# Kernel optimization log

Hardware: AMD Instinct MI355X
Metric: run time of the kernel (lower is better)

## Reference

```python
import jax, jax.numpy as jnp
import numpy as np

E, H, F = 1024, 16, 4096
WH, WW = 32, 32
B = 4
L = WH * WW           # 1024 cross-attn kv tokens
N = L + 1             # 1025 decoder tokens (CLS + window)
D = E // H
SCALE = D ** -0.5
NEG = -1e9            # stands in for -inf in the causal mask


def _rel_coords(Wh, Ww):
    coords = np.stack(np.meshgrid(np.arange(Wh), np.arange(Ww), indexing='ij')).reshape(2, -1)
    rc = (coords[:, :, None] - coords[:, None, :]).transpose(1, 2, 0).astype(np.int64)
    rc[:, :, 0] += Wh - 1
    rc[:, :, 1] += Ww - 1
    rc[:, :, 0] *= 2 * Ww - 1
    return rc.sum(-1)  # (L, L)


def rel_index_self(Wh, Ww):
    nrd = (2 * Wh - 1) * (2 * Ww - 1) + 3
    l = Wh * Ww
    idx = np.zeros((l + 1, l + 1), dtype=np.int32)
    idx[1:, 1:] = _rel_coords(Wh, Ww)
    idx[0, :] = nrd - 3
    idx[:, 0] = nrd - 2
    idx[0, 0] = nrd - 1
    return idx


def rel_index_cross(Wh, Ww):
    nrd = (2 * Wh - 1) * (2 * Ww - 1) + 1
    l = Wh * Ww
    idx = np.zeros((l + 1, l), dtype=np.int32)
    idx[1:, :] = _rel_coords(Wh, Ww)
    idx[0, :] = nrd - 1
    return idx


IDX_SELF = jnp.asarray(rel_index_self(WH, WW))    # (N, N) int32
IDX_CROSS = jnp.asarray(rel_index_cross(WH, WW))  # (N, L) int32
CAUSAL = jnp.triu(jnp.full((N, N), NEG, jnp.float32), 1)


def _ln(x, g, b, eps=1e-5):
    m = x.mean(-1, keepdims=True)
    v = ((x - m) ** 2).mean(-1, keepdims=True)
    return (x - m) * jax.lax.rsqrt(v + eps) * g + b


def setup_inputs():
    key = jax.random.key(0)
    ks = jax.random.split(key, 24)
    g = lambda i, shape, s=0.02: jax.random.normal(ks[i], shape, jnp.float32) * s
    return dict(
        x=g(0, (B, N, E), 1.0),
        y=g(1, (B, L, E), 1.0),
        norm1_g=jnp.ones((E,), jnp.float32), norm1_b=jnp.zeros((E,), jnp.float32),
        norm2_g=jnp.ones((E,), jnp.float32), norm2_b=jnp.zeros((E,), jnp.float32),
        norm3_g=jnp.ones((E,), jnp.float32), norm3_b=jnp.zeros((E,), jnp.float32),
        sa_qkv_w=g(2, (3 * E, E)),
        sa_q_bias=g(3, (E,)),
        sa_v_bias=g(4, (E,)),
        sa_rpb=g(5, ((2 * WH - 1) * (2 * WW - 1) + 3, H)),
        sa_proj_w=g(6, (E, E)), sa_proj_b=g(7, (E,)),
        ca_q_w=g(8, (E, E)),
        ca_kv_w=g(9, (2 * E, E)),
        ca_q_bias=g(10, (E,)),
        ca_v_bias=g(11, (E,)),
        ca_rpb=g(12, ((2 * WH - 1) * (2 * WW - 1) + 1, H)),
        ca_proj_w=g(13, (E, E)), ca_proj_b=g(14, (E,)),
        fc1_w=g(15, (F, E)), fc1_b=g(16, (F,)),
        fc2_w=g(17, (E, F)), fc2_b=g(18, (E,)),
        gamma1=jnp.full((E,), 0.1, jnp.float32),
        gamma2=jnp.full((E,), 0.1, jnp.float32),
        gamma3=jnp.full((E,), 0.1, jnp.float32),
    )


def reference(x, y, norm1_g, norm1_b, norm2_g, norm2_b, norm3_g, norm3_b,
              sa_qkv_w, sa_q_bias, sa_v_bias, sa_rpb, sa_proj_w, sa_proj_b,
              ca_q_w, ca_kv_w, ca_q_bias, ca_v_bias, ca_rpb, ca_proj_w, ca_proj_b,
              fc1_w, fc1_b, fc2_w, fc2_b, gamma1, gamma2, gamma3):
    # cross_attn.extract_kv(y): k gets zero bias, v gets v_bias
    kv_bias = jnp.concatenate([jnp.zeros((E,), x.dtype), ca_v_bias])
    kv = (y @ ca_kv_w.T + kv_bias).reshape(B, L, 2, H, D)
    ck = kv[:, :, 0].transpose(0, 2, 1, 3)  # (B,H,L,D)
    cv = kv[:, :, 1].transpose(0, 2, 1, 3)

    # --- causal self-attention with gathered relative-position bias ---
    h = _ln(x, norm1_g, norm1_b)
    qkv_bias = jnp.concatenate([sa_q_bias, jnp.zeros((E,), x.dtype), sa_v_bias])
    qkv = (h @ sa_qkv_w.T + qkv_bias).reshape(B, N, 3, H, D)
    q = qkv[:, :, 0].transpose(0, 2, 1, 3) * SCALE  # (B,H,N,D)
    k = qkv[:, :, 1].transpose(0, 2, 1, 3)
    v = qkv[:, :, 2].transpose(0, 2, 1, 3)
    bias = sa_rpb[IDX_SELF].transpose(2, 0, 1) + CAUSAL  # (H,N,N)
    attn = jnp.einsum('bhqd,bhkd->bhqk', q, k) + bias[None]
    attn = jax.nn.softmax(attn, axis=-1)
    sa = jnp.einsum('bhqk,bhkd->bhqd', attn, v).transpose(0, 2, 1, 3).reshape(B, N, E)
    sa = sa @ sa_proj_w.T + sa_proj_b
    x = x + gamma1 * sa

    # --- cross-attention with gathered relative-position bias ---
    h = _ln(x, norm2_g, norm2_b)
    q = (h @ ca_q_w.T + ca_q_bias).reshape(B, N, H, D).transpose(0, 2, 1, 3) * SCALE
    cbias = ca_rpb[IDX_CROSS].transpose(2, 0, 1)  # (H,N,L)
    attn = jnp.einsum('bhqd,bhkd->bhqk', q, ck) + cbias[None]
    attn = jax.nn.softmax(attn, axis=-1)
    ca = jnp.einsum('bhqk,bhkd->bhqd', attn, cv).transpose(0, 2, 1, 3).reshape(B, N, E)
    ca = ca @ ca_proj_w.T + ca_proj_b
    x = x + gamma2 * ca

    # --- FFN (Linear -> GELU -> Linear, no inner identity) ---
    h = _ln(x, norm3_g, norm3_b)
    h = jax.nn.gelu(h @ fc1_w.T + fc1_b, approximate=False)
    h = h @ fc2_w.T + fc2_b
    x = x + gamma3 * h
    return x
```

## Files before the change

### kernel.cpp

```cpp
#include <hip/hip_runtime.h>
#include <hip/hip_bf16.h>
#include <math.h>

typedef __bf16 bf16;
typedef __bf16 bf16x8 __attribute__((ext_vector_type(8)));
typedef float f32x4 __attribute__((ext_vector_type(4)));

#define MP    4224
#define MACT  4100
#define NQTOK 1025
#define NKTOK 1024
#define EDIM  1024
#define FDIM  4096
#define NHEAD 16
#define HD    64
#define QSCALE 0.125f
#define VTS   1056

__device__ __forceinline__ void glds16(const bf16* g, bf16* l) {
  __builtin_amdgcn_global_load_lds(
      (const __attribute__((address_space(1))) void*)g,
      (__attribute__((address_space(3))) void*)l, 16, 0, 0);
}

__device__ __forceinline__ bf16x8 ld8(const void* p, size_t i, bool f32) {
  if (f32) {
    const float* q = (const float*)p + i;
    bf16x8 r;
#pragma unroll
    for (int j = 0; j < 8; ++j) r[j] = (bf16)q[j];
    return r;
  }
  return *(const bf16x8*)((const bf16*)p + i);
}

struct WPtrs { const float* s[8]; };
__global__ __launch_bounds__(256) void conv_kernel(WPtrs wp, bf16* dst) {
  const size_t sz[8] = {3145728UL, 1048576UL, 1048576UL, 2097152UL,
                        1048576UL, 4194304UL, 4194304UL, 4194304UL};
  size_t id = ((size_t)blockIdx.x * 256 + threadIdx.x) * 8;
  size_t off = 0;
#pragma unroll
  for (int i = 0; i < 8; ++i) {
    if (id < off + sz[i]) {
      const float* s = wp.s[i] + (id - off);
      bf16x8 r;
#pragma unroll
      for (int j = 0; j < 8; ++j) r[j] = (bf16)s[j];
      *(bf16x8*)(dst + id) = r;
      return;
    }
    off += sz[i];
  }
}

__global__ void zero_pads_kernel(bf16* hln) {
  int i = blockIdx.x * 256 + threadIdx.x;
  const int n = (MP - MACT) * EDIM;
  if (i < n) hln[(size_t)MACT * EDIM + i] = (bf16)0.0f;
}

template<bool FIRST>
__global__ __launch_bounds__(256) void ln_kernel(const float* __restrict__ src,
    float* __restrict__ xf, bf16* __restrict__ out,
    const float* __restrict__ g, const float* __restrict__ bta) {
  const int row = blockIdx.x;
  const int tid = threadIdx.x;
  float v[4];
#pragma unroll
  for (int i = 0; i < 4; ++i) {
    v[i] = src[(size_t)row * EDIM + tid + i * 256];
    if (FIRST) xf[(size_t)row * EDIM + tid + i * 256] = v[i];
  }
  float s = 0.f, sq = 0.f;
#pragma unroll
  for (int i = 0; i < 4; ++i) { s += v[i]; sq += v[i] * v[i]; }
#pragma unroll
  for (int m = 32; m >= 1; m >>= 1) {
    s += __shfl_xor(s, m);
    sq += __shfl_xor(sq, m);
  }
  __shared__ float ss[4], ssq[4];
  const int wave = tid >> 6;
  if ((tid & 63) == 0) { ss[wave] = s; ssq[wave] = sq; }
  __syncthreads();
  s = ss[0] + ss[1] + ss[2] + ss[3];
  sq = ssq[0] + ssq[1] + ssq[2] + ssq[3];
  const float mean = s * (1.f / EDIM);
  const float var = sq * (1.f / EDIM) - mean * mean;
  const float rstd = rsqrtf(var + 1e-5f);
#pragma unroll
  for (int i = 0; i < 4; ++i) {
    int e = tid + i * 256;
    out[(size_t)row * EDIM + e] = (bf16)((v[i] - mean) * rstd * g[e] + bta[e]);
  }
}

__global__ __launch_bounds__(256) void fc2_reduce_kernel(
    const float* __restrict__ p0, const float* __restrict__ xf,
    const float* __restrict__ bias, const float* __restrict__ gamma,
    float* __restrict__ outf) {
  size_t i = ((size_t)blockIdx.x * 256 + threadIdx.x) * 4;
  if (i >= (size_t)MACT * EDIM) return;
  f32x4 a = *(const f32x4*)(p0 + i);
  f32x4 b = *(const f32x4*)(outf + i);
  f32x4 x = *(const f32x4*)(xf + i);
  const int gn = (int)(i & (EDIM - 1));
  f32x4 r;
#pragma unroll
  for (int j = 0; j < 4; ++j)
    r[j] = x[j] + gamma[gn + j] * (a[j] + b[j] + bias[gn + j]);
  *(f32x4*)(outf + i) = r;
}

enum { EPI_QKV = 0, EPI_KV = 1, EPI_Q = 2, EPI_RES = 3, EPI_GELU = 4,
       EPI_FINAL = 5, EPI_PART = 6 };

template<int EPI, bool ASY>
__global__ __launch_bounds__(256) void gemm_bt(
    const void* __restrict__ A, const void* __restrict__ Bw,
    int K, int Kc,
    const float* __restrict__ bias0, const float* __restrict__ bias1,
    const float* __restrict__ gamma, float* __restrict__ xf,
    bf16* __restrict__ out0, bf16* __restrict__ out1, bf16* __restrict__ out2,
    float* __restrict__ outf)
{
  constexpr int LDP = ASY ? 32 : 40;
  __shared__ bf16 As[128][LDP];
  __shared__ bf16 Bs[128][LDP];
  const int tid = threadIdx.x;
  const int lane = tid & 63, wave = tid >> 6;
  const int quad = lane >> 4, l16 = lane & 15;
  const int wr = wave >> 1, wc = wave & 1;
  const int m0 = blockIdx.y * 128, n0 = blockIdx.x * 128;
  const int kbase = blockIdx.z * Kc;
  const bool first = (blockIdx.z == 0);
  const int r0 = tid >> 2, c0 = (tid & 3) * 8;

  const bf16* gA = nullptr; const bf16* gB = nullptr;
  bf16* lA = nullptr; bf16* lB = nullptr;
  if (ASY) {
    gA = (const bf16*)A + (size_t)(m0 + wave * 16 + (lane >> 2)) * K + kbase + (lane & 3) * 8;
    gB = (const bf16*)Bw + (size_t)(n0 + wave * 16 + (lane >> 2)) * K + kbase + (lane & 3) * 8;
    lA = &As[wave * 16][0];
    lB = &Bs[wave * 16][0];
  }

  f32x4 acc[4][4];
#pragma unroll
  for (int i = 0; i < 4; ++i)
#pragma unroll
    for (int j = 0; j < 4; ++j)
#pragma unroll
      for (int r = 0; r < 4; ++r) acc[i][j][r] = 0.f;

  for (int k0 = 0; k0 < Kc; k0 += 32) {
    if (ASY) {
      glds16(gA, lA);
      glds16(gA + (size_t)64 * K, lA + 64 * 32);
      glds16(gB, lB);
      glds16(gB + (size_t)64 * K, lB + 64 * 32);
      gA += 32; gB += 32;
    } else {
      const bool f32a = (EPI == EPI_KV);
      const size_t kk = (size_t)(kbase + k0);
      *(bf16x8*)(&As[r0][c0])      = ld8(A,  (size_t)(m0 + r0) * K + kk + c0, f32a);
      *(bf16x8*)(&As[r0 + 64][c0]) = ld8(A,  (size_t)(m0 + r0 + 64) * K + kk + c0, f32a);
      *(bf16x8*)(&Bs[r0][c0])      = ld8(Bw, (size_t)(n0 + r0) * K + kk + c0, true);
      *(bf16x8*)(&Bs[r0 + 64][c0]) = ld8(Bw, (size_t)(n0 + r0 + 64) * K + kk + c0, true);
    }
    __syncthreads();
    bf16x8 af[4], bfv[4];
#pragma unroll
    for (int i = 0; i < 4; ++i) {
      af[i]  = *(const bf16x8*)(&As[wr * 64 + i * 16 + l16][quad * 8]);
      bfv[i] = *(const bf16x8*)(&Bs[wc * 64 + i * 16 + l16][quad * 8]);
    }
#pragma unroll
    for (int mb = 0; mb < 4; ++mb)
#pragma unroll
      for (int nb = 0; nb < 4; ++nb)
        acc[mb][nb] = __builtin_amdgcn_mfma_f32_16x16x32_bf16(af[mb], bfv[nb], acc[mb][nb], 0, 0, 0);
    __syncthreads();
  }

#pragma unroll
  for (int mb = 0; mb < 4; ++mb) {
#pragma unroll
    for (int r = 0; r < 4; ++r) {
      const int gm = m0 + wr * 64 + mb * 16 + quad * 4 + r;
#pragma unroll
      for (int nb = 0; nb < 4; ++nb) {
        const int gn = n0 + wc * 64 + nb * 16 + l16;
        float v = acc[mb][nb][r];
        if (EPI == EPI_QKV) {
          if (gm < MACT) {
            unsigned b = (unsigned)gm / 1025u;
            unsigned t = (unsigned)gm - b * 1025u;
            int sec = gn >> 10, e = gn & 1023;
            int h = e >> 6, d = e & 63;
            if (sec == 0)
              out0[((size_t)(b * NHEAD + h) * NQTOK + t) * HD + d] =
                  (bf16)((v + bias0[e]) * QSCALE);
            else if (sec == 1)
              out1[((size_t)(b * NHEAD + h) * NQTOK + t) * HD + d] = (bf16)v;
            else
              out2[((size_t)(b * NHEAD + h) * HD + d) * VTS + t] =
                  (bf16)(v + bias1[e]);
          }
        } else if (EPI == EPI_KV) {
          unsigned b = (unsigned)gm >> 10;
          unsigned t = (unsigned)gm & 1023u;
          int sec = gn >> 10, e = gn & 1023;
          int h = e >> 6, d = e & 63;
          if (sec == 0)
            out0[((size_t)(b * NHEAD + h) * NKTOK + t) * HD + d] = (bf16)v;
          else
            out1[((size_t)(b * NHEAD + h) * HD + d) * NKTOK + t] =
                (bf16)(v + bias1[e]);
        } else if (EPI == EPI_Q) {
          if (gm < MACT) {
            unsigned b = (unsigned)gm / 1025u;
            unsigned t = (unsigned)gm - b * 1025u;
            int h = gn >> 6, d = gn & 63;
            outf[((size_t)(b * NHEAD + h) * NQTOK + t) * HD + d] =
                (v + bias0[gn]) * QSCALE;
          }
        } else if (EPI == EPI_RES) {
          if (gm < MACT) {
            size_t o = (size_t)gm * EDIM + gn;
            xf[o] += gamma[gn] * (v + bias0[gn]);
          }
        } else if (EPI == EPI_GELU) {
          float z = v + bias0[gn];
          float ge = 0.5f * z * (1.0f + erff(z * 0.70710678118f));
          out0[(size_t)gm * FDIM + gn] = (bf16)ge;
        } else if (EPI == EPI_PART) {
          if (gm < MACT) {
            float* dst = first ? xf : outf;
            dst[(size_t)gm * EDIM + gn] = v;
          }
        } else {
          if (gm < MACT) {
            size_t o = (size_t)gm * EDIM + gn;
            float add = gamma[gn] * (v + (first ? bias0[gn] : 0.f));
            if (first) add += xf[o];
            atomicAdd(&outf[o], add);
          }
        }
      }
    }
  }
}

template<bool CROSS>
__global__ __launch_bounds__(256) void attn_kernel(
    const void* __restrict__ Q, const bf16* __restrict__ Kg,
    const bf16* __restrict__ Vg, const float* __restrict__ rpb,
    bf16* __restrict__ out)
{
  const int NK  = CROSS ? NKTOK : NQTOK;
  const int NRD = CROSS ? 3970 : 3972;
  const int VS  = CROSS ? NKTOK : VTS;
  const int qt  = CROSS ? blockIdx.x : (16 - blockIdx.x);
  const int h = blockIdx.y, b = blockIdx.z;
  const int tid = threadIdx.x;
  const int lane = tid & 63, wave = tid >> 6;
  const int quad = lane >> 4, l16 = lane & 15;

  __shared__ bf16 rpb_s[4096];
  __shared__ bf16 Ks[64][72];
  __shared__ bf16 Vt[64][72];

  for (int i = tid; i < 4096; i += 256)
    rpb_s[i] = (bf16)((i < NRD) ? rpb[(size_t)i * NHEAD + h] : 0.f);

  const int q0 = qt * 64;
  const int qrow = q0 + wave * 16 + l16;
  const size_t qhb = (size_t)(b * NHEAD + h) * NQTOK;
  bf16x8 qf0, qf1;
  if (qrow < NQTOK) {
    if (CROSS) {
      const float* Qf = (const float*)Q + (qhb + qrow) * HD;
#pragma unroll
      for (int j = 0; j < 8; ++j) {
        qf0[j] = (bf16)Qf[quad * 8 + j];
        qf1[j] = (bf16)Qf[32 + quad * 8 + j];
      }
    } else {
      const bf16* Qb = (const bf16*)Q;
      qf0 = *(const bf16x8*)(Qb + (qhb + qrow) * HD + quad * 8);
      qf1 = *(const bf16x8*)(Qb + (qhb + qrow) * HD + 32 + quad * 8);
    }
  } else {
#pragma unroll
    for (int j = 0; j < 8; ++j) { qf0[j] = (bf16)0.f; qf1[j] = (bf16)0.f; }
  }

  const int qg = qrow;
  const int qp = qg - 1;
  const int qcode = (qg > 0) ? ((qp >> 5) * 63 + (qp & 31) + 1984) : 0;

  float m_run = -1e30f, l_run = 0.f;
  f32x4 oacc[4];
#pragma unroll
  for (int d = 0; d < 4; ++d)
#pragma unroll
    for (int r = 0; r < 4; ++r) oacc[d][r] = 0.f;

  const size_t kvbK = (size_t)(b * NHEAD + h) * NK;
  const size_t vbase = (size_t)(b * NHEAD + h) * HD;
  const int nch = CROSS ? (NKTOK / 64) : (qt + 1);

  const int rr = tid >> 3;
  const int co = (tid & 7) * 8;

  const int srcA = (quad & 1) * 32 + l16;
  const int srcB = srcA + 16;

  bf16x8 krg[2], vrg[2];
  auto stage_load = [&](int c) {
    const int kc = c * 64;
#pragma unroll
    for (int vv = 0; vv < 2; ++vv) {
      const int row = rr + vv * 32;
      if (!CROSS && kc + row >= NK) {
#pragma unroll
        for (int j = 0; j < 8; ++j) krg[vv][j] = (bf16)0.f;
      } else {
        krg[vv] = *(const bf16x8*)(Kg + (kvbK + kc + row) * HD + co);
      }
      if (!CROSS && kc + co >= NK) {
#pragma unroll
        for (int j = 0; j < 8; ++j) vrg[vv][j] = (bf16)0.f;
      } else {
        vrg[vv] = *(const bf16x8*)(Vg + (vbase + row) * VS + kc + co);
      }
    }
  };

  stage_load(0);
  for (int c = 0; c < nch; ++c) {
    const int kc = c * 64;
    if (c) __syncthreads();
#pragma unroll
    for (int vv = 0; vv < 2; ++vv) {
      const int row = rr + vv * 32;
      *(bf16x8*)(&Ks[row][co]) = krg[vv];
      *(bf16x8*)(&Vt[row][co]) = vrg[vv];
    }
    __syncthreads();
    if (c + 1 < nch) stage_load(c + 1);

    float sv[4][4];
#pragma unroll
    for (int kb = 0; kb < 4; ++kb) {
      f32x4 a;
#pragma unroll
      for (int r = 0; r < 4; ++r) a[r] = 0.f;
      bf16x8 kf0 = *(const bf16x8*)(&Ks[kb * 16 + l16][quad * 8]);
      bf16x8 kf1 = *(const bf16x8*)(&Ks[kb * 16 + l16][32 + quad * 8]);
      a = __builtin_amdgcn_mfma_f32_16x16x32_bf16(kf0, qf0, a, 0, 0, 0);
      a = __builtin_amdgcn_mfma_f32_16x16x32_bf16(kf1, qf1, a, 0, 0, 0);
#pragma unroll
      for (int r = 0; r < 4; ++r) {
        const int kg = kc + kb * 16 + quad * 4 + r;
        int kcode;
        if (CROSS) kcode = (kg >> 5) * 63 + (kg & 31);
        else {
          int k1 = kg - 1;
          kcode = (kg > 0) ? ((k1 >> 5) * 63 + (k1 & 31)) : 0;
        }
        bool valid = CROSS ? true : (kg < NK && kg <= qg);
        int idx;
        if (CROSS) {
          idx = (qg == 0) ? 3969 : (qcode - kcode);
        } else {
          idx = (qg == 0) ? ((kg == 0) ? 3971 : 3969)
                          : ((kg == 0) ? 3970 : (qcode - kcode));
        }
        idx &= 4095;
        sv[kb][r] = valid ? (a[r] + (float)rpb_s[idx]) : -1e30f;
      }
    }

    float mx = sv[0][0];
#pragma unroll
    for (int kb = 0; kb < 4; ++kb)
#pragma unroll
      for (int r = 0; r < 4; ++r) mx = fmaxf(mx, sv[kb][r]);
    mx = fmaxf(mx, __shfl_xor(mx, 16));
    mx = fmaxf(mx, __shfl_xor(mx, 32));

    if (!__all(mx - m_run <= 8.f)) {
      const float mnew = fmaxf(m_run, mx);
      const float alpha = __expf(m_run - mnew);
      m_run = mnew;
      l_run *= alpha;
      float alr[4];
#pragma unroll
      for (int r = 0; r < 4; ++r) alr[r] = __shfl(alpha, quad * 4 + r);
#pragma unroll
      for (int d = 0; d < 4; ++d)
#pragma unroll
        for (int r = 0; r < 4; ++r) oacc[d][r] *= alr[r];
    }

    float rs = 0.f;
    unsigned pk[4][2];
#pragma unroll
    for (int kb = 0; kb < 4; ++kb) {
      float p0 = __expf(sv[kb][0] - m_run);
      float p1 = __expf(sv[kb][1] - m_run);
      float p2 = __expf(sv[kb][2] - m_run);
      float p3 = __expf(sv[kb][3] - m_run);
      rs += (p0 + p1) + (p2 + p3);
      union { __bf16 h[2]; unsigned u; } w0, w1;
      w0.h[0] = (bf16)p0; w0.h[1] = (bf16)p1;
      w1.h[0] = (bf16)p2; w1.h[1] = (bf16)p3;
      pk[kb][0] = w0.u; pk[kb][1] = w1.u;
    }
    rs += __shfl_xor(rs, 16);
    rs += __shfl_xor(rs, 32);
    l_run += rs;

    union { unsigned u[4]; bf16x8 v; } f0, f1;
#pragma unroll
    for (int p = 0; p < 4; ++p) {
      const int src = (p < 2) ? srcA : srcB;
      unsigned a0 = (unsigned)__shfl((int)pk[0][p & 1], src);
      unsigned a1 = (unsigned)__shfl((int)pk[1][p & 1], src);
      unsigned b0 = (unsigned)__shfl((int)pk[2][p & 1], src);
      unsigned b1 = (unsigned)__shfl((int)pk[3][p & 1], src);
      f0.u[p] = (quad < 2) ? a0 : a1;
      f1.u[p] = (quad < 2) ? b0 : b1;
    }

#pragma unroll
    for (int db = 0; db < 4; ++db) {
      bf16x8 vf0 = *(const bf16x8*)(&Vt[db * 16 + l16][quad * 8]);
      bf16x8 vf1 = *(const bf16x8*)(&Vt[db * 16 + l16][32 + quad * 8]);
      oacc[db] = __builtin_amdgcn_mfma_f32_16x16x32_bf16(f0.v, vf0, oacc[db], 0, 0, 0);
      oacc[db] = __builtin_amdgcn_mfma_f32_16x16x32_bf16(f1.v, vf1, oacc[db], 0, 0, 0);
    }
  }

#pragma unroll
  for (int r = 0; r < 4; ++r) {
    const int qo = q0 + wave * 16 + quad * 4 + r;
    if (qo < NQTOK) {
      const float inv = 1.f / __shfl(l_run, quad * 4 + r);
      const size_t row = (size_t)b * NQTOK + qo;
#pragma unroll
      for (int db = 0; db < 4; ++db)
        out[row * EDIM + h * HD + db * 16 + l16] = (bf16)(oacc[db][r] * inv);
    }
  }
}

extern "C" void kernel_launch(void* const* d_in, const int* in_sizes, int n_in,
                              void* d_out, int out_size, void* d_ws, size_t ws_size,
                              hipStream_t stream) {
  (void)in_sizes; (void)n_in; (void)out_size;
  const float* x        = (const float*)d_in[0];
  const float* y        = (const float*)d_in[1];
  const float* n1g      = (const float*)d_in[2];
  const float* n1b      = (const float*)d_in[3];
  const float* n2g      = (const float*)d_in[4];
  const float* n2b      = (const float*)d_in[5];
  const float* n3g      = (const float*)d_in[6];
  const float* n3b      = (const float*)d_in[7];
  const float* sa_qkv_w = (const float*)d_in[8];
  const float* sa_qb    = (const float*)d_in[9];
  const float* sa_vb    = (const float*)d_in[10];
  const float* sa_rpb   = (const float*)d_in[11];
  const float* sa_pw    = (const float*)d_in[12];
  const float* sa_pb    = (const float*)d_in[13];
  const float* ca_qw    = (const float*)d_in[14];
  const float* ca_kvw   = (const float*)d_in[15];
  const float* ca_qb    = (const float*)d_in[16];
  const float* ca_vb    = (const float*)d_in[17];
  const float* ca_rpb   = (const float*)d_in[18];
  const float* ca_pw    = (const float*)d_in[19];
  const float* ca_pb    = (const float*)d_in[20];
  const float* fc1_w    = (const float*)d_in[21];
  const float* fc1_b    = (const float*)d_in[22];
  const float* fc2_w    = (const float*)d_in[23];
  const float* fc2_b    = (const float*)d_in[24];
  const float* g1       = (const float*)d_in[25];
  const float* g2       = (const float*)d_in[26];
  const float* g3       = (const float*)d_in[27];
  float* outf = (float*)d_out;
  float* qtf  = (float*)d_out;

  char* w = (char*)d_ws;
  float* xf = (float*)w;  w += (size_t)MP * EDIM * 4;
  bf16* hln = (bf16*)w;   w += (size_t)MP * EDIM * 2;
  char* big = w;          w += (size_t)MP * FDIM * 2;
  const size_t qkv_sz = (size_t)4 * NHEAD * NQTOK * HD * 2;
  bf16* qt = (bf16*)big;
  bf16* kt = (bf16*)(big + qkv_sz);
  bf16* vt = (bf16*)(big + 2 * qkv_sz);
  bf16* h1 = (bf16*)big;
  bf16* wpool = (bf16*)w; w += 20971520UL * 2;
  const bool asy = ((size_t)(w - (char*)d_ws) <= ws_size);

  bf16* qkvw_b = wpool;
  bf16* pw_b   = qkvw_b + 3145728UL;
  bf16* cqw_b  = pw_b   + 1048576UL;
  bf16* ckvw_b = cqw_b  + 1048576UL;
  bf16* cpw_b  = ckvw_b + 2097152UL;
  bf16* fc1w_b = cpw_b  + 1048576UL;
  bf16* fc2w_b = fc1w_b + 4194304UL;
  bf16* y_b    = fc2w_b + 4194304UL;
  float* part0 = (float*)wpool;

  if (asy) {
    WPtrs wp = {{sa_qkv_w, sa_pw, ca_qw, ca_kvw, ca_pw, fc1_w, fc2_w, y}};
    conv_kernel<<<10240, 256, 0, stream>>>(wp, wpool);
  }
  zero_pads_kernel<<<dim3(((MP - MACT) * EDIM + 255) / 256), 256, 0, stream>>>(hln);

  ln_kernel<true><<<MACT, 256, 0, stream>>>(x, xf, hln, n1g, n1b);
  if (asy) gemm_bt<EPI_QKV, true><<<dim3(24, 33, 1), 256, 0, stream>>>(hln, qkvw_b, 1024, 1024,
      sa_qb, sa_vb, nullptr, nullptr, qt, kt, vt, nullptr);
  else     gemm_bt<EPI_QKV, false><<<dim3(24, 33, 1), 256, 0, stream>>>(hln, sa_qkv_w, 1024, 1024,
      sa_qb, sa_vb, nullptr, nullptr, qt, kt, vt, nullptr);
  attn_kernel<false><<<dim3(17, NHEAD, 4), 256, 0, stream>>>(qt, kt, vt, sa_rpb, hln);
  if (asy) gemm_bt<EPI_RES, true><<<dim3(8, 33, 1), 256, 0, stream>>>(hln, pw_b, 1024, 1024,
      sa_pb, nullptr, g1, xf, nullptr, nullptr, nullptr, nullptr);
  else     gemm_bt<EPI_RES, false><<<dim3(8, 33, 1), 256, 0, stream>>>(hln, sa_pw, 1024, 1024,
      sa_pb, nullptr, g1, xf, nullptr, nullptr, nullptr, nullptr);

  ln_kernel<false><<<MACT, 256, 0, stream>>>(xf, nullptr, hln, n2g, n2b);
  if (asy) gemm_bt<EPI_Q, true><<<dim3(8, 33, 1), 256, 0, stream>>>(hln, cqw_b, 1024, 1024,
      ca_qb, nullptr, nullptr, nullptr, nullptr, nullptr, nullptr, qtf);
  else     gemm_bt<EPI_Q, false><<<dim3(8, 33, 1), 256, 0, stream>>>(hln, ca_qw, 1024, 1024,
      ca_qb, nullptr, nullptr, nullptr, nullptr, nullptr, nullptr, qtf);
  if (asy) gemm_bt<EPI_KV, true><<<dim3(16, 32, 1), 256, 0, stream>>>(y_b, ckvw_b, 1024, 1024,
      nullptr, ca_vb, nullptr, nullptr, kt, vt, nullptr, nullptr);
  else     gemm_bt<EPI_KV, false><<<dim3(16, 32, 1), 256, 0, stream>>>(y, ca_kvw, 1024, 1024,
      nullptr, ca_vb, nullptr, nullptr, kt, vt, nullptr, nullptr);
  attn_kernel<true><<<dim3(17, NHEAD, 4), 256, 0, stream>>>(qtf, kt, vt, ca_rpb, hln);
  if (asy) gemm_bt<EPI_RES, true><<<dim3(8, 33, 1), 256, 0, stream>>>(hln, cpw_b, 1024, 1024,
      ca_pb, nullptr, g2, xf, nullptr, nullptr, nullptr, nullptr);
  else     gemm_bt<EPI_RES, false><<<dim3(8, 33, 1), 256, 0, stream>>>(hln, ca_pw, 1024, 1024,
      ca_pb, nullptr, g2, xf, nullptr, nullptr, nullptr, nullptr);

  ln_kernel<false><<<MACT, 256, 0, stream>>>(xf, nullptr, hln, n3g, n3b);
  if (asy) gemm_bt<EPI_GELU, true><<<dim3(32, 33, 1), 256, 0, stream>>>(hln, fc1w_b, 1024, 1024,
      fc1_b, nullptr, nullptr, nullptr, h1, nullptr, nullptr, nullptr);
  else     gemm_bt<EPI_GELU, false><<<dim3(32, 33, 1), 256, 0, stream>>>(hln, fc1_w, 1024, 1024,
      fc1_b, nullptr, nullptr, nullptr, h1, nullptr, nullptr, nullptr);
  if (asy) {
    gemm_bt<EPI_PART, true><<<dim3(8, 33, 2), 256, 0, stream>>>(h1, fc2w_b, 4096, 2048,
        nullptr, nullptr, nullptr, part0, nullptr, nullptr, nullptr, outf);
    fc2_reduce_kernel<<<dim3(4100), 256, 0, stream>>>(part0, xf, fc2_b, g3, outf);
  } else {
    hipMemsetAsync(outf, 0, (size_t)MACT * EDIM * 4, stream);
    gemm_bt<EPI_FINAL, false><<<dim3(8, 33, 4), 256, 0, stream>>>(h1, fc2_w, 4096, 1024,
        fc2_b, nullptr, g3, xf, nullptr, nullptr, nullptr, outf);
  }
}
```

Baseline: 719.7 us.

## Double-buffer GEMM LDS tiles and precompute attention bias indices

The GEMM kernel now keeps two LDS tile buffers and issues the next k-slice load before computing on the current one, which removes one barrier per iteration and overlaps global loads with MFMA work. In the attention kernel, the relative-position bias indices are computed once per thread and then shifted by a constant per chunk, and the causal validity check runs only on the last chunk. s_setprio calls are also placed around the MFMA sections. The double buffer doubles GEMM LDS use, which may lower occupancy. The async global_load_lds path now writes into the next buffer without waiting for completion before the following barrier, which risks hazards.

```diff
diff --git a/kernel.cpp b/kernel.cpp
--- a/kernel.cpp
+++ b/kernel.cpp
@@ -126,8 +126,8 @@
     float* __restrict__ outf)
 {
   constexpr int LDP = ASY ? 32 : 40;
-  __shared__ bf16 As[128][LDP];
-  __shared__ bf16 Bs[128][LDP];
+  __shared__ bf16 As[2][128][LDP];
+  __shared__ bf16 Bs[2][128][LDP];
   const int tid = threadIdx.x;
   const int lane = tid & 63, wave = tid >> 6;
   const int quad = lane >> 4, l16 = lane & 15;
@@ -138,43 +138,49 @@
   const int r0 = tid >> 2, c0 = (tid & 3) * 8;
 
   const bf16* gA = nullptr; const bf16* gB = nullptr;
-  bf16* lA = nullptr; bf16* lB = nullptr;
   if (ASY) {
     gA = (const bf16*)A + (size_t)(m0 + wave * 16 + (lane >> 2)) * K + kbase + (lane & 3) * 8;
     gB = (const bf16*)Bw + (size_t)(n0 + wave * 16 + (lane >> 2)) * K + kbase + (lane & 3) * 8;
-    lA = &As[wave * 16][0];
-    lB = &Bs[wave * 16][0];
-  }
-
-  f32x4 acc[4][4];
-#pragma unroll
-  for (int i = 0; i < 4; ++i)
-#pragma unroll
-    for (int j = 0; j < 4; ++j)
-#pragma unroll
-      for (int r = 0; r < 4; ++r) acc[i][j][r] = 0.f;
-
-  for (int k0 = 0; k0 < Kc; k0 += 32) {
+  }
+
+  auto stage = [&](int bi, int kk) {
     if (ASY) {
-      glds16(gA, lA);
-      glds16(gA + (size_t)64 * K, lA + 64 * 32);
-      glds16(gB, lB);
-      glds16(gB + (size_t)64 * K, lB + 64 * 32);
-      gA += 32; gB += 32;
+      const bf16* pA = gA + kk;
+      const bf16* pB = gB + kk;
+      bf16* la = &As[bi][wave * 16][0];
+      bf16* lb = &Bs[bi][wave * 16][0];
+      glds16(pA, la);
+      glds16(pA + (size_t)64 * K, la + 64 * LDP);
+      glds16(pB, lb);
+      glds16(pB + (size_t)64 * K, lb + 64 * LDP);
     } else {
       const bool f32a = (EPI == EPI_KV);
-      const size_t kk = (size_t)(kbase + k0);
-      *(bf16x8*)(&As[r0][c0])      = ld8(A,  (size_t)(m0 + r0) * K + kk + c0, f32a);
-      *(bf16x8*)(&As[r0 + 64][c0]) = ld8(A,  (size_t)(m0 + r0 + 64) * K + kk + c0, f32a);
-      *(bf16x8*)(&Bs[r0][c0])      = ld8(Bw, (size_t)(n0 + r0) * K + kk + c0, true);
-      *(bf16x8*)(&Bs[r0 + 64][c0]) = ld8(Bw, (size_t)(n0 + r0 + 64) * K + kk + c0, true);
-    }
-    __syncthreads();
+      const size_t kkk = (size_t)(kbase + kk);
+      *(bf16x8*)(&As[bi][r0][c0])      = ld8(A,  (size_t)(m0 + r0) * K + kkk + c0, f32a);
+      *(bf16x8*)(&As[bi][r0 + 64][c0]) = ld8(A,  (size_t)(m0 + r0 + 64) * K + kkk + c0, f32a);
+      *(bf16x8*)(&Bs[bi][r0][c0])      = ld8(Bw, (size_t)(n0 + r0) * K + kkk + c0, true);
+      *(bf16x8*)(&Bs[bi][r0 + 64][c0]) = ld8(Bw, (size_t)(n0 + r0 + 64) * K + kkk + c0, true);
+    }
+  };
+
+  f32x4 acc[4][4];
+#pragma unroll
+  for (int i = 0; i < 4; ++i)
+#pragma unroll
+    for (int j = 0; j < 4; ++j)
+#pragma unroll
+      for (int r = 0; r < 4; ++r) acc[i][j][r] = 0.f;
+
+  stage(0, 0);
+  __syncthreads();
+  int buf = 0;
+  for (int k0 = 0; k0 < Kc; k0 += 32) {
+    if (k0 + 32 < Kc) stage(buf ^ 1, k0 + 32);
     bf16x8 af[4], bfv[4];
 #pragma unroll
     for (int i = 0; i < 4; ++i) {
-      af[i]  = *(const bf16x8*)(&As[wr * 64 + i * 16 + l16][quad * 8]);
-      bfv[i] = *(const bf16x8*)(&Bs[wc * 64 + i * 16 + l16][quad * 8]);
+      af[i]  = *(const bf16x8*)(&As[buf][wr * 64 + i * 16 + l16][quad * 8]);
+      bfv[i] = *(const bf16x8*)(&Bs[buf][wc * 64 + i * 16 + l16][quad * 8]);
     }
 #pragma unroll
     for (int mb = 0; mb < 4; ++mb)
@@ -182,6 +188,7 @@
       for (int nb = 0; nb < 4; ++nb)
         acc[mb][nb] = __builtin_amdgcn_mfma_f32_16x16x32_bf16(af[mb], bfv[nb], acc[mb][nb], 0, 0, 0);
     __syncthreads();
+    buf ^= 1;
   }
 
 #pragma unroll
@@ -301,6 +308,18 @@
   const int qp = qg - 1;
   const int qcode = (qg > 0) ? ((qp >> 5) * 63 + (qp & 31) + 1984) : 0;
 
+  int ib[4][4];
+#pragma unroll
+  for (int kb = 0; kb < 4; ++kb)
+#pragma unroll
+    for (int r = 0; r < 4; ++r) {
+      const int o = kb * 16 + quad * 4 + r;
+      const int om = CROSS ? o : (o - 1);
+      const int ocode = (om >> 5) * 63 + (om & 31);
+      ib[kb][r] = qcode - ocode;
+    }
+  const bool q0cls = (q0 == 0);
+
   float m_run = -1e30f, l_run = 0.f;
   f32x4 oacc[4];
 #pragma unroll
@@ -340,6 +359,7 @@
   };
 
   stage_load(0);
+  int c126 = 0;
   for (int c = 0; c < nch; ++c) {
     const int kc = c * 64;
     if (c) __syncthreads();
@@ -352,37 +372,54 @@
     __syncthreads();
     if (c + 1 < nch) stage_load(c + 1);
 
-    float sv[4][4];
+    f32x4 aacc[4];
+    __builtin_amdgcn_s_setprio(1);
 #pragma unroll
     for (int kb = 0; kb < 4; ++kb) {
-      f32x4 a;
-#pragma unroll
-      for (int r = 0; r < 4; ++r) a[r] = 0.f;
       bf16x8 kf0 = *(const bf16x8*)(&Ks[kb * 16 + l16][quad * 8]);
       bf16x8 kf1 = *(const bf16x8*)(&Ks[kb * 16 + l16][32 + quad * 8]);
+      f32x4 a;
+#pragma unroll
+      for (int r = 0; r < 4; ++r) a[r] = 0.f;
       a = __builtin_amdgcn_mfma_f32_16x16x32_bf16(kf0, qf0, a, 0, 0, 0);
       a = __builtin_amdgcn_mfma_f32_16x16x32_bf16(kf1, qf1, a, 0, 0, 0);
-#pragma unroll
-      for (int r = 0; r < 4; ++r) {
-        const int kg = kc + kb * 16 + quad * 4 + r;
-        int kcode;
-        if (CROSS) kcode = (kg >> 5) * 63 + (kg & 31);
-        else {
-          int k1 = kg - 1;
-          kcode = (kg > 0) ? ((k1 >> 5) * 63 + (k1 & 31)) : 0;
+      aacc[kb] = a;
+    }
+    __builtin_amdgcn_s_setprio(0);
+
+    float sv[4][4];
+    const bool lastc = (!CROSS) && (c == nch - 1);
+    const bool firstc = (c == 0);
+    if (!lastc) {
+#pragma unroll
+      for (int kb = 0; kb < 4; ++kb)
+#pragma unroll
+        for (int r = 0; r < 4; ++r) {
+          int idx = ib[kb][r] - c126;
+          if (q0cls) { if (qg == 0) idx = 3969; }
+          if (!CROSS && firstc && kb == 0 && r == 0) {
+            if (quad == 0) idx = (qg == 0) ? 3971 : 3970;
+          }
+          idx &= 4095;
+          sv[kb][r] = aacc[kb][r] + (float)rpb_s[idx];
         }
-        bool valid = CROSS ? true : (kg < NK && kg <= qg);
-        int idx;
-        if (CROSS) {
-          idx = (qg == 0) ? 3969 : (qcode - kcode);
-        } else {
-          idx = (qg == 0) ? ((kg == 0) ? 3971 : 3969)
-                          : ((kg == 0) ? 3970 : (qcode - kcode));
+    } else {
+#pragma unroll
+      for (int kb = 0; kb < 4; ++kb)
+#pragma unroll
+        for (int r = 0; r < 4; ++r) {
+          int idx = ib[kb][r] - c126;
+          if (q0cls) { if (qg == 0) idx = 3969; }
+          if (firstc && kb == 0 && r == 0) {
+            if (quad == 0) idx = (qg == 0) ? 3971 : 3970;
+          }
+          idx &= 4095;
+          const int kg = kc + kb * 16 + quad * 4 + r;
+          const bool valid = (kg < NK) && (kg <= qg);
+          sv[kb][r] = valid ? (aacc[kb][r] + (float)rpb_s[idx]) : -1e30f;
         }
-        idx &= 4095;
-        sv[kb][r] = valid ? (a[r] + (float)rpb_s[idx]) : -1e30f;
-      }
-    }
+    }
+    c126 += 126;
 
     float mx = sv[0][0];
 #pragma unroll
@@ -436,6 +473,7 @@
       f1.u[p] = (quad < 2) ? b0 : b1;
     }
 
+    __builtin_amdgcn_s_setprio(1);
 #pragma unroll
     for (int db = 0; db < 4; ++db) {
       bf16x8 vf0 = *(const bf16x8*)(&Vt[db * 16 + l16][quad * 8]);
@@ -443,6 +481,7 @@
       oacc[db] = __builtin_amdgcn_mfma_f32_16x16x32_bf16(f0.v, vf0, oacc[db], 0, 0, 0);
       oacc[db] = __builtin_amdgcn_mfma_f32_16x16x32_bf16(f1.v, vf1, oacc[db], 0, 0, 0);
     }
+    __builtin_amdgcn_s_setprio(0);
   }
 
 #pragma unroll
```

Result: faster. 678.5 us (-5.7%).
